# Performance work log

Hardware: AMD Instinct MI355X
Metric: run time of the kernel (lower is better)

The kernel has to match this reference:

```python
import jax, jax.numpy as jnp
import numpy as np

B, T, D = 2, 2048, 2048
H, KV, HD = 16, 4, 128
EPS = 1e-6


def _rmsnorm(x, scale):
    # flax.linen.RMSNorm over last axis: x / sqrt(mean(x^2) + eps) * scale
    var = jnp.mean(jnp.square(x), axis=-1, keepdims=True)
    return x * jax.lax.rsqrt(var + EPS) * scale


def _rope(x, cos, sin):
    # x: [b, t, h, d]; cos/sin: [t, d]
    x_rot = jnp.stack([-x[..., 1::2], x[..., 0::2]], axis=-1)
    x_rot = x_rot.reshape(*x_rot.shape[:-2], -1)
    return x * cos[None, :, None, :] + x_rot * sin[None, :, None, :]


def setup_inputs() -> dict:
    key = jax.random.key(0)
    ks = jax.random.split(key, 5)
    x = jax.random.normal(ks[0], (B, T, D), jnp.float32)
    Wq = jax.random.normal(ks[1], (D, H * HD), jnp.float32) / np.sqrt(D)
    Wk = jax.random.normal(ks[2], (D, KV * HD), jnp.float32) / np.sqrt(D)
    Wv = jax.random.normal(ks[3], (D, KV * HD), jnp.float32) / np.sqrt(D)
    Wo = jax.random.normal(ks[4], (H * HD, D), jnp.float32) / np.sqrt(H * HD)
    q_scale = jnp.ones((HD,), jnp.float32)
    k_scale = jnp.ones((HD,), jnp.float32)
    # standard RoPE tables, interleaved-pair convention
    pos = jnp.arange(T, dtype=jnp.float32)
    inv_freq = 1.0 / (10000.0 ** (jnp.arange(0, HD, 2, dtype=jnp.float32) / HD))
    freqs = pos[:, None] * inv_freq[None, :]  # [T, HD/2]
    cos = jnp.repeat(jnp.cos(freqs), 2, axis=-1)  # [T, HD]
    sin = jnp.repeat(jnp.sin(freqs), 2, axis=-1)
    mask = jnp.tril(jnp.ones((T, T), bool))[None, None]  # causal [1,1,T,T]
    return {"x": x, "Wq": Wq, "Wk": Wk, "Wv": Wv, "Wo": Wo,
            "q_scale": q_scale, "k_scale": k_scale,
            "cos": cos, "sin": sin, "mask": mask}


def reference(x, Wq, Wk, Wv, Wo, q_scale, k_scale, cos, sin, mask):
    num_groups = H // KV
    q = (x @ Wq).reshape(B, T, H, HD)
    k = (x @ Wk).reshape(B, T, KV, HD)
    v = (x @ Wv).reshape(B, T, KV, HD)
    q = _rmsnorm(q, q_scale)
    k = _rmsnorm(k, k_scale)
    q = _rope(q, cos, sin)
    k = _rope(k, cos, sin)
    k = jnp.repeat(k, num_groups, axis=2)  # [b, t, H, d]
    v = jnp.repeat(v, num_groups, axis=2)
    scores = jnp.einsum('bqhd,bkhd->bhqk', q, k) / jnp.sqrt(jnp.float32(HD))
    scores = jnp.where(mask, scores, jnp.finfo(scores.dtype).min)
    attn = jax.nn.softmax(scores, axis=-1)
    out = jnp.einsum('bhqk,bkhd->bqhd', attn, v)
    out = out.reshape(B, T, H * HD)
    return out @ Wo
```

## Files before the change

### kernel.cpp

```cpp
#include <hip/hip_runtime.h>
#include <hip/hip_bf16.h>

#define B_   2
#define T_   2048
#define D_   2048
#define H_   16
#define KV_  4
#define HD_  128
#define BT_  (B_*T_)
#define QKVP 3072
#define KOFF 2048
#define VOFF 2560
static constexpr float EPS_ = 1e-6f;

typedef unsigned short u16;
typedef __attribute__((ext_vector_type(8))) short short8;
typedef __attribute__((ext_vector_type(4))) float f32x4;
typedef __attribute__((ext_vector_type(4))) unsigned short u16x4;

__device__ __forceinline__ u16 f2bf(float f){
    unsigned u = __float_as_uint(f);
    u += 0x7FFF + ((u >> 16) & 1);
    return (u16)(u >> 16);
}
__device__ __forceinline__ float bf2f(u16 u){
    return __uint_as_float((unsigned)u << 16);
}

__device__ __forceinline__ void async_copy16(const void* g, void* l) {
    __builtin_amdgcn_global_load_lds(
        (const __attribute__((address_space(1))) unsigned int*)g,
        (__attribute__((address_space(3))) unsigned int*)l, 16, 0, 0);
}

__global__ __launch_bounds__(256) void cvt_f32_bf16_kernel(
    const float* __restrict__ in, u16* __restrict__ out, int n)
{
    const int i = (blockIdx.x*256 + threadIdx.x)*4;
    if (i < n) {
        float4 v = *(const float4*)&in[i];
        u16x4 w = { f2bf(v.x), f2bf(v.y), f2bf(v.z), f2bf(v.w) };
        *(u16x4*)&out[i] = w;
    }
}

__global__ __launch_bounds__(256) void transpose_cvt_kernel(
    const float* __restrict__ in, u16* __restrict__ out, int R, int C)
{
    __shared__ u16 tile[64][65];
    const int r0 = blockIdx.y*64, c0 = blockIdx.x*64;
    const int tr = threadIdx.x >> 4;
    const int tc = (threadIdx.x & 15) * 4;
    #pragma unroll
    for (int i = 0; i < 4; i++) {
        const int r = tr + i*16;
        float4 v = *(const float4*)&in[(size_t)(r0 + r)*C + c0 + tc];
        tile[tc+0][r] = f2bf(v.x);
        tile[tc+1][r] = f2bf(v.y);
        tile[tc+2][r] = f2bf(v.z);
        tile[tc+3][r] = f2bf(v.w);
    }
    __syncthreads();
    #pragma unroll
    for (int i = 0; i < 4; i++) {
        const int c = tr + i*16;
        u16x4 w = { tile[c][tc+0], tile[c][tc+1], tile[c][tc+2], tile[c][tc+3] };
        *(u16x4*)&out[(size_t)(c0 + c)*R + r0 + tc] = w;
    }
}

__global__ __launch_bounds__(256) void transpose_v_kernel(
    const u16* __restrict__ qkv, u16* __restrict__ vt)
{
    __shared__ u16 tile[64][65];
    const int t0 = blockIdx.x*64;
    const int d0 = blockIdx.y*64;
    const int bk = blockIdx.z;
    const int tr = threadIdx.x >> 4;
    const int tc = (threadIdx.x & 15) * 4;
    #pragma unroll
    for (int i = 0; i < 4; i++) {
        const int t = t0 + tr + i*16;
        u16x4 v = *(const u16x4*)&qkv[(size_t)((bk>>2)*T_ + t)*QKVP + VOFF
                                      + (bk&3)*HD_ + d0 + tc];
        tile[tc+0][tr+i*16] = v[0];
        tile[tc+1][tr+i*16] = v[1];
        tile[tc+2][tr+i*16] = v[2];
        tile[tc+3][tr+i*16] = v[3];
    }
    __syncthreads();
    #pragma unroll
    for (int i = 0; i < 4; i++) {
        const int d = tr + i*16;
        u16x4 w = { tile[d][tc+0], tile[d][tc+1], tile[d][tc+2], tile[d][tc+3] };
        *(u16x4*)&vt[((size_t)bk*HD_ + d0 + d)*T_ + t0 + tc] = w;
    }
}

#define GBM 128
#define GBN 128
#define GBK 32

template<bool OUT_BF16>
__global__ __launch_bounds__(256) void gemm_mfma_kernel(
    const u16* __restrict__ A, const u16* __restrict__ Bt,
    void* __restrict__ C, int N, int K, int lda, int ldb, int ldc)
{
    __shared__ __align__(16) u16 As[GBM][GBK];
    __shared__ __align__(16) u16 Bs[GBN][GBK];
    const int tid  = threadIdx.x;
    const int lane = tid & 63;
    const int wave = tid >> 6;
    const int l15  = lane & 15;
    const int quad = lane >> 4;
    const int wr   = (wave >> 1) * 64;
    const int wc   = (wave & 1) * 64;
    const size_t row0 = (size_t)blockIdx.y * GBM;
    const size_t col0 = (size_t)blockIdx.x * GBN;

    f32x4 acc[4][4];
    #pragma unroll
    for (int i = 0; i < 4; i++)
        #pragma unroll
        for (int j = 0; j < 4; j++)
            acc[i][j] = (f32x4){0.f,0.f,0.f,0.f};

    for (int k0 = 0; k0 < K; k0 += GBK) {
        #pragma unroll
        for (int c = 0; c < 2; c++) {
            const int e = (c*256 + tid) * 8;
            const int r = e >> 5, cc = e & 31;
            async_copy16(A  + (row0 + r)*lda + k0 + cc, &As[r][cc]);
            async_copy16(Bt + (col0 + r)*ldb + k0 + cc, &Bs[r][cc]);
        }
        __syncthreads();

        short8 af[4], bf[4];
        #pragma unroll
        for (int i = 0; i < 4; i++)
            af[i] = *(const short8*)&As[wr + i*16 + l15][quad*8];
        #pragma unroll
        for (int j = 0; j < 4; j++)
            bf[j] = *(const short8*)&Bs[wc + j*16 + l15][quad*8];
        #pragma unroll
        for (int i = 0; i < 4; i++)
            #pragma unroll
            for (int j = 0; j < 4; j++)
                acc[i][j] = __builtin_amdgcn_mfma_f32_16x16x32_bf16(
                    af[i], bf[j], acc[i][j], 0, 0, 0);
        __syncthreads();
    }

    #pragma unroll
    for (int i = 0; i < 4; i++)
        #pragma unroll
        for (int r = 0; r < 4; r++) {
            const size_t row = row0 + wr + i*16 + quad*4 + r;
            #pragma unroll
            for (int j = 0; j < 4; j++) {
                const size_t col = col0 + wc + j*16 + l15;
                if (OUT_BF16) ((u16*)C)[row*ldc + col] = f2bf(acc[i][j][r]);
                else          ((float*)C)[row*ldc + col] = acc[i][j][r];
            }
        }
}

__global__ __launch_bounds__(256) void rmsnorm_rope_kernel(
    u16* __restrict__ qk, const float* __restrict__ scale,
    const float* __restrict__ cosT, const float* __restrict__ sinT,
    int heads_per_token, int head_off, float post_scale)
{
    const int wid   = blockIdx.x*4 + (threadIdx.x >> 6);
    const int lane  = threadIdx.x & 63;
    const int token = wid / heads_per_token;
    const int hidx  = wid % heads_per_token;
    const int t     = token & (T_ - 1);
    u16* p = qk + (size_t)token*QKVP + head_off + hidx*HD_ + lane*2;

    const unsigned u = *(const unsigned*)p;
    const float x0 = bf2f((u16)(u & 0xffff));
    const float x1 = bf2f((u16)(u >> 16));
    float ss = x0*x0 + x1*x1;
    #pragma unroll
    for (int off = 32; off > 0; off >>= 1) ss += __shfl_xor(ss, off);
    const float rms = rsqrtf(ss * (1.0f/HD_) + EPS_);

    const float2 sc = *(const float2*)&scale[lane*2];
    const float2 cs = *(const float2*)&cosT[(size_t)t*HD_ + lane*2];
    const float2 sn = *(const float2*)&sinT[(size_t)t*HD_ + lane*2];
    const float n0 = x0 * rms * sc.x;
    const float n1 = x1 * rms * sc.y;
    const float r0 = (n0*cs.x - n1*sn.x) * post_scale;
    const float r1 = (n1*cs.y + n0*sn.y) * post_scale;
    *(unsigned*)p = (unsigned)f2bf(r0) | ((unsigned)f2bf(r1) << 16);
}

#define BQ2 128
#define BKV 64

__global__ __launch_bounds__(256, 2) void attn_mfma12_kernel(
    const u16* __restrict__ qkv, const u16* __restrict__ Vtg)
{
    __shared__ __align__(16) u16 Ks[2][16][BKV][8];
    __shared__ __align__(16) u16 Vt[2][8][HD_][8];
    __shared__ __align__(16) u16 Pb[4][2][8][16][8];

    const int x    = blockIdx.x;
    const int h    = blockIdx.y;
    const int b    = blockIdx.z;
    const int qt   = b ? x : 15 - x;
    const int kvh  = h >> 2;
    const int tid  = threadIdx.x;
    const int lane = tid & 63;
    const int wave = tid >> 6;
    const int l15  = lane & 15;
    const int quad = lane >> 4;
    const int q0   = qt * BQ2;
    const int ntiles = 2*qt + 2;

    short8 qf[2][4];
    #pragma unroll
    for (int rf = 0; rf < 2; rf++) {
        const u16* qbase = qkv + (size_t)(b*T_ + q0 + rf*64 + wave*16 + l15)*QKVP + h*HD_;
        #pragma unroll
        for (int kt = 0; kt < 4; kt++)
            qf[rf][kt] = *(const short8*)(qbase + kt*32 + quad*8);
    }

    float lsum[2][4];
    #pragma unroll
    for (int rf = 0; rf < 2; rf++)
        #pragma unroll
        for (int r = 0; r < 4; r++) lsum[rf][r] = 0.f;
    f32x4 oacc[2][8];
    #pragma unroll
    for (int rf = 0; rf < 2; rf++)
        #pragma unroll
        for (int cv = 0; cv < 8; cv++) oacc[rf][cv] = (f32x4){0.f,0.f,0.f,0.f};

    #pragma unroll
    for (int it = 0; it < 4; it++) {
        const int n2  = it*256 + tid;
        const int cc  = n2 >> 6;
        const int key = n2 & 63;
        async_copy16(qkv + (size_t)(b*T_ + key)*QKVP + KOFF + kvh*HD_ + cc*8,
                     &Ks[0][cc][key][0]);
    }
    #pragma unroll
    for (int it = 0; it < 4; it++) {
        const int n2 = it*256 + tid;
        const int cc = n2 >> 7;
        const int d  = n2 & 127;
        async_copy16(Vtg + ((size_t)(b*KV_ + kvh)*HD_ + d)*T_ + cc*8,
                     &Vt[0][cc][d][0]);
    }
    __syncthreads();

    int cur = 0;
    for (int t = 0; t < ntiles; t++) {
        if (t + 1 < ntiles) {
            const int k0n = (t + 1) * BKV;
            #pragma unroll
            for (int it = 0; it < 4; it++) {
                const int n2  = it*256 + tid;
                const int cc  = n2 >> 6;
                const int key = n2 & 63;
                async_copy16(qkv + (size_t)(b*T_ + k0n + key)*QKVP + KOFF + kvh*HD_ + cc*8,
                             &Ks[cur^1][cc][key][0]);
            }
            #pragma unroll
            for (int it = 0; it < 4; it++) {
                const int n2 = it*256 + tid;
                const int cc = n2 >> 7;
                const int d  = n2 & 127;
                async_copy16(Vtg + ((size_t)(b*KV_ + kvh)*HD_ + d)*T_ + k0n + cc*8,
                             &Vt[cur^1][cc][d][0]);
            }
        }

        const int k0 = t * BKV;

        f32x4 s[2][4];
        #pragma unroll
        for (int rf = 0; rf < 2; rf++)
            #pragma unroll
            for (int c = 0; c < 4; c++) s[rf][c] = (f32x4){0.f,0.f,0.f,0.f};
        __builtin_amdgcn_s_setprio(1);
        #pragma unroll
        for (int kt = 0; kt < 4; kt++) {
            #pragma unroll
            for (int c = 0; c < 4; c++) {
                short8 kf = *(const short8*)&Ks[cur][kt*4 + quad][c*16 + l15][0];
                #pragma unroll
                for (int rf = 0; rf < 2; rf++)
                    s[rf][c] = __builtin_amdgcn_mfma_f32_16x16x32_bf16(
                        qf[rf][kt], kf, s[rf][c], 0, 0, 0);
            }
        }
        __builtin_amdgcn_s_setprio(0);

        if (t >= ntiles - 2) {
            #pragma unroll
            for (int rf = 0; rf < 2; rf++) {
                const int qrow0 = q0 + rf*64 + wave*16 + quad*4;
                #pragma unroll
                for (int r = 0; r < 4; r++)
                    #pragma unroll
                    for (int c = 0; c < 4; c++) {
                        const int key = k0 + c*16 + l15;
                        if (key > qrow0 + r) s[rf][c][r] = -1e30f;
                    }
            }
        }
        #pragma unroll
        for (int rf = 0; rf < 2; rf++)
            #pragma unroll
            for (int r = 0; r < 4; r++)
                #pragma unroll
                for (int c = 0; c < 4; c++) {
                    const float p = __expf(s[rf][c][r]);
                    lsum[rf][r] += p;
                    Pb[wave][rf][c*2 + (l15 >> 3)][quad*4 + r][l15 & 7] = f2bf(p);
                }

        __builtin_amdgcn_s_setprio(1);
        #pragma unroll
        for (int kt2 = 0; kt2 < 2; kt2++) {
            short8 pa[2];
            #pragma unroll
            for (int rf = 0; rf < 2; rf++)
                pa[rf] = *(const short8*)&Pb[wave][rf][kt2*4 + quad][l15][0];
            #pragma unroll
            for (int cv = 0; cv < 8; cv++) {
                short8 vf = *(const short8*)&Vt[cur][kt2*4 + quad][cv*16 + l15][0];
                #pragma unroll
                for (int rf = 0; rf < 2; rf++)
                    oacc[rf][cv] = __builtin_amdgcn_mfma_f32_16x16x32_bf16(
                        pa[rf], vf, oacc[rf][cv], 0, 0, 0);
            }
        }
        __builtin_amdgcn_s_setprio(0);

        __syncthreads();
        cur ^= 1;
    }

    #pragma unroll
    for (int rf = 0; rf < 2; rf++)
        #pragma unroll
        for (int r = 0; r < 4; r++) {
            float tot = lsum[rf][r];
            #pragma unroll
            for (int off = 1; off < 16; off <<= 1)
                tot += __shfl_xor(tot, off, 16);
            const float linv = 1.0f / tot;
            u16* orow = (u16*)qkv + (size_t)(b*T_ + q0 + rf*64 + wave*16 + quad*4 + r)*QKVP
                        + h*HD_ + l15;
            #pragma unroll
            for (int cv = 0; cv < 8; cv++)
                orow[cv*16] = f2bf(oacc[rf][cv][r] * linv);
        }
}

extern "C" void kernel_launch(void* const* d_in, const int* in_sizes, int n_in,
                              void* d_out, int out_size, void* d_ws, size_t ws_size,
                              hipStream_t stream)
{
    const float* x    = (const float*)d_in[0];
    const float* Wq   = (const float*)d_in[1];
    const float* Wk   = (const float*)d_in[2];
    const float* Wv   = (const float*)d_in[3];
    const float* Wo   = (const float*)d_in[4];
    const float* qsc  = (const float*)d_in[5];
    const float* ksc  = (const float*)d_in[6];
    const float* cosT = (const float*)d_in[7];
    const float* sinT = (const float*)d_in[8];
    float* out = (float*)d_out;

    u16* xb     = (u16*)d_ws;
    u16* Wqkvt  = xb    + (size_t)BT_*D_;
    u16* Wot    = Wqkvt + (size_t)QKVP*D_;
    u16* qkv    = Wot   + (size_t)D_*(H_*HD_);
    u16* vtg    = qkv   + (size_t)BT_*QKVP;

    cvt_f32_bf16_kernel<<<(BT_*D_)/1024, 256, 0, stream>>>(x, xb, BT_*D_);
    transpose_cvt_kernel<<<dim3((H_*HD_)/64,  D_/64), 256, 0, stream>>>(
        Wq, Wqkvt, D_, H_*HD_);
    transpose_cvt_kernel<<<dim3((KV_*HD_)/64, D_/64), 256, 0, stream>>>(
        Wk, Wqkvt + (size_t)KOFF*D_, D_, KV_*HD_);
    transpose_cvt_kernel<<<dim3((KV_*HD_)/64, D_/64), 256, 0, stream>>>(
        Wv, Wqkvt + (size_t)VOFF*D_, D_, KV_*HD_);
    transpose_cvt_kernel<<<dim3(D_/64, (H_*HD_)/64),  256, 0, stream>>>(
        Wo, Wot, H_*HD_, D_);

    gemm_mfma_kernel<true><<<dim3(QKVP/GBN, BT_/GBM), 256, 0, stream>>>(
        xb, Wqkvt, qkv, QKVP, D_, D_, D_, QKVP);

    rmsnorm_rope_kernel<<<(BT_*H_)/4,  256, 0, stream>>>(
        qkv, qsc, cosT, sinT, H_, 0, 0.08838834764831845f);
    rmsnorm_rope_kernel<<<(BT_*KV_)/4, 256, 0, stream>>>(
        qkv, ksc, cosT, sinT, KV_, KOFF, 1.0f);

    transpose_v_kernel<<<dim3(T_/64, HD_/64, B_*KV_), 256, 0, stream>>>(qkv, vtg);

    attn_mfma12_kernel<<<dim3(T_/BQ2, H_, B_), 256, 0, stream>>>(qkv, vtg);

    gemm_mfma_kernel<false><<<dim3(D_/GBN, BT_/GBM), 256, 0, stream>>>(
        qkv, Wot, out, D_, D_, QKVP, D_, D_);
}
```

Before: 380.1 us.

## Split long causal query tiles across two KV halves with combine pass

The eight longest causal query tiles per head are each split into two blocks, one per half of the KV range. Each half writes unnormalized fp32 partial outputs and row sums, and a new combine kernel adds the halves, normalizes and writes bf16. The goal is to shorten the critical path of the attention grid and improve load balance across CUs. The cost is an extra launch plus fp32 partial traffic, staged in the output buffer and the x-bf16 workspace. Plain summation of the halves is only correct because the softmax uses a fixed max rather than a running one.

```diff
diff --git a/kernel.cpp b/kernel.cpp
--- a/kernel.cpp
+++ b/kernel.cpp
@@ -197,18 +197,35 @@
 
 #define BQ2 128
 #define BKV 64
-
-__global__ __launch_bounds__(256, 2) void attn_mfma12_kernel(
-    const u16* __restrict__ qkv, const u16* __restrict__ Vtg)
+#define QSPLIT   8
+#define NSPL     8
+#define POTILE   (128*128)
+
+__global__ __launch_bounds__(256, 2) void attn_mfma13_kernel(
+    const u16* __restrict__ qkv, const u16* __restrict__ Vtg,
+    float* __restrict__ partO, float* __restrict__ psum)
 {
     __shared__ __align__(16) u16 Ks[2][16][BKV][8];
     __shared__ __align__(16) u16 Vt[2][8][HD_][8];
     __shared__ __align__(16) u16 Pb[4][2][8][16][8];
 
-    const int x    = blockIdx.x;
+    const int xb2  = blockIdx.x;
     const int h    = blockIdx.y;
     const int b    = blockIdx.z;
-    const int qt   = b ? x : 15 - x;
+    int qt, t0, t1, half;
+    bool full;
+    if (xb2 < 2*NSPL) {
+        qt   = 15 - (xb2 >> 1);
+        half = xb2 & 1;
+        t0   = half ? (qt + 1) : 0;
+        t1   = half ? (2*qt + 2) : (qt + 1);
+        full = false;
+    } else {
+        qt   = 23 - xb2;
+        t0   = 0; t1 = 2*qt + 2; half = 0;
+        full = true;
+    }
+
     const int kvh  = h >> 2;
     const int tid  = threadIdx.x;
     const int lane = tid & 63;
@@ -216,7 +233,6 @@
     const int l15  = lane & 15;
     const int quad = lane >> 4;
     const int q0   = qt * BQ2;
-    const int ntiles = 2*qt + 2;
 
     short8 qf[2][4];
     #pragma unroll
@@ -238,27 +254,30 @@
         #pragma unroll
         for (int cv = 0; cv < 8; cv++) oacc[rf][cv] = (f32x4){0.f,0.f,0.f,0.f};
 
-    #pragma unroll
-    for (int it = 0; it < 4; it++) {
-        const int n2  = it*256 + tid;
-        const int cc  = n2 >> 6;
-        const int key = n2 & 63;
-        async_copy16(qkv + (size_t)(b*T_ + key)*QKVP + KOFF + kvh*HD_ + cc*8,
-                     &Ks[0][cc][key][0]);
-    }
-    #pragma unroll
-    for (int it = 0; it < 4; it++) {
-        const int n2 = it*256 + tid;
-        const int cc = n2 >> 7;
-        const int d  = n2 & 127;
-        async_copy16(Vtg + ((size_t)(b*KV_ + kvh)*HD_ + d)*T_ + cc*8,
-                     &Vt[0][cc][d][0]);
+    {
+        const int k00 = t0 * BKV;
+        #pragma unroll
+        for (int it = 0; it < 4; it++) {
+            const int n2  = it*256 + tid;
+            const int cc  = n2 >> 6;
+            const int key = n2 & 63;
+            async_copy16(qkv + (size_t)(b*T_ + k00 + key)*QKVP + KOFF + kvh*HD_ + cc*8,
+                         &Ks[0][cc][key][0]);
+        }
+        #pragma unroll
+        for (int it = 0; it < 4; it++) {
+            const int n2 = it*256 + tid;
+            const int cc = n2 >> 7;
+            const int d  = n2 & 127;
+            async_copy16(Vtg + ((size_t)(b*KV_ + kvh)*HD_ + d)*T_ + k00 + cc*8,
+                         &Vt[0][cc][d][0]);
+        }
     }
     __syncthreads();
 
     int cur = 0;
-    for (int t = 0; t < ntiles; t++) {
-        if (t + 1 < ntiles) {
+    for (int t = t0; t < t1; t++) {
+        if (t + 1 < t1) {
             const int k0n = (t + 1) * BKV;
             #pragma unroll
             for (int it = 0; it < 4; it++) {
@@ -299,7 +318,7 @@
         }
         __builtin_amdgcn_s_setprio(0);
 
-        if (t >= ntiles - 2) {
+        if (t >= 2*qt) {
             #pragma unroll
             for (int rf = 0; rf < 2; rf++) {
                 const int qrow0 = q0 + rf*64 + wave*16 + quad*4;
@@ -345,21 +364,71 @@
         cur ^= 1;
     }
 
-    #pragma unroll
-    for (int rf = 0; rf < 2; rf++)
-        #pragma unroll
-        for (int r = 0; r < 4; r++) {
-            float tot = lsum[rf][r];
-            #pragma unroll
-            for (int off = 1; off < 16; off <<= 1)
-                tot += __shfl_xor(tot, off, 16);
-            const float linv = 1.0f / tot;
-            u16* orow = (u16*)qkv + (size_t)(b*T_ + q0 + rf*64 + wave*16 + quad*4 + r)*QKVP
-                        + h*HD_ + l15;
-            #pragma unroll
-            for (int cv = 0; cv < 8; cv++)
-                orow[cv*16] = f2bf(oacc[rf][cv][r] * linv);
-        }
+    if (full) {
+        #pragma unroll
+        for (int rf = 0; rf < 2; rf++)
+            #pragma unroll
+            for (int r = 0; r < 4; r++) {
+                float tot = lsum[rf][r];
+                #pragma unroll
+                for (int off = 1; off < 16; off <<= 1)
+                    tot += __shfl_xor(tot, off, 16);
+                const float linv = 1.0f / tot;
+                u16* orow = (u16*)qkv + (size_t)(b*T_ + q0 + rf*64 + wave*16 + quad*4 + r)*QKVP
+                            + h*HD_ + l15;
+                #pragma unroll
+                for (int cv = 0; cv < 8; cv++)
+                    orow[cv*16] = f2bf(oacc[rf][cv][r] * linv);
+            }
+    } else {
+        const int hidx = ((b*H_ + h)*NSPL + (qt - QSPLIT))*2 + half;
+        float* po = partO + (size_t)hidx*POTILE;
+        float* ps = psum  + (size_t)hidx*128;
+        #pragma unroll
+        for (int rf = 0; rf < 2; rf++)
+            #pragma unroll
+            for (int r = 0; r < 4; r++) {
+                float tot = lsum[rf][r];
+                #pragma unroll
+                for (int off = 1; off < 16; off <<= 1)
+                    tot += __shfl_xor(tot, off, 16);
+                const int row = rf*64 + wave*16 + quad*4 + r;
+                #pragma unroll
+                for (int cv = 0; cv < 8; cv++)
+                    po[row*128 + cv*16 + l15] = oacc[rf][cv][r];
+                if (l15 == 0) ps[row] = tot;
+            }
+    }
+}
+
+__global__ __launch_bounds__(256) void attn_combine_kernel(
+    const float* __restrict__ partO, const float* __restrict__ psum,
+    u16* __restrict__ qkv)
+{
+    const int p  = blockIdx.x;
+    const int qt = QSPLIT + (p & 7);
+    const int bh = p >> 3;
+    const int h  = bh & 15;
+    const int b  = bh >> 4;
+    const int base = ((b*H_ + h)*NSPL + (qt - QSPLIT))*2;
+    const float* p0 = partO + (size_t)(base + 0)*POTILE;
+    const float* p1 = partO + (size_t)(base + 1)*POTILE;
+    const float* s0 = psum  + (size_t)(base + 0)*128;
+    const float* s1 = psum  + (size_t)(base + 1)*128;
+    const int tid = threadIdx.x;
+    const int row = tid >> 1;
+    const int c0  = (tid & 1) * 64;
+    const float linv = 1.0f / (s0[row] + s1[row]);
+    u16* orow = qkv + (size_t)(b*T_ + qt*BQ2 + row)*QKVP + h*HD_;
+    #pragma unroll
+    for (int d = 0; d < 64; d += 4) {
+        const int col = c0 + d;
+        u16x4 w = { f2bf((p0[row*128 + col+0] + p1[row*128 + col+0]) * linv),
+                    f2bf((p0[row*128 + col+1] + p1[row*128 + col+1]) * linv),
+                    f2bf((p0[row*128 + col+2] + p1[row*128 + col+2]) * linv),
+                    f2bf((p0[row*128 + col+3] + p1[row*128 + col+3]) * linv) };
+        *(u16x4*)&orow[col] = w;
+    }
 }
 
 extern "C" void kernel_launch(void* const* d_in, const int* in_sizes, int n_in,
@@ -382,6 +451,8 @@
     u16* Wot    = Wqkvt + (size_t)QKVP*D_;
     u16* qkv    = Wot   + (size_t)D_*(H_*HD_);
     u16* vtg    = qkv   + (size_t)BT_*QKVP;
+    float* partO = out;
+    float* psum  = (float*)xb;
 
     cvt_f32_bf16_kernel<<<(BT_*D_)/1024, 256, 0, stream>>>(x, xb, BT_*D_);
     transpose_cvt_kernel<<<dim3((H_*HD_)/64,  D_/64), 256, 0, stream>>>(
@@ -403,7 +474,10 @@
 
     transpose_v_kernel<<<dim3(T_/64, HD_/64, B_*KV_), 256, 0, stream>>>(qkv, vtg);
 
-    attn_mfma12_kernel<<<dim3(T_/BQ2, H_, B_), 256, 0, stream>>>(qkv, vtg);
+    attn_mfma13_kernel<<<dim3(2*NSPL + QSPLIT, H_, B_), 256, 0, stream>>>(
+        qkv, vtg, partO, psum);
+
+    attn_combine_kernel<<<B_*H_*NSPL, 256, 0, stream>>>(partO, psum, qkv);
 
     gemm_mfma_kernel<false><<<dim3(D_/GBN, BT_/GBM), 256, 0, stream>>>(
         qkv, Wot, out, D_, D_, QKVP, D_, D_);
```

After: 398.3 us. 1.05x slower.

## Enlarge attention query tile to 256 rows with 8 waves and XOR-swizzled LDS

Applied to the files above, without the earlier changes.

The attention kernel now processes 256 query rows per block using 512 threads (8 waves), so each staged K/V tile is reused by twice as many queries. The K and V shared-memory layouts are changed to a row-major form with an XOR swizzle on the 16-byte chunk index, meant to avoid LDS bank conflicts on the fragment reads. The balanced reordering of query tiles across batches is dropped, and the grid halves to 256 blocks at one block per CU. This raises the causal tail imbalance and lowers occupancy in exchange for less K/V load traffic.

```diff
diff --git a/kernel.cpp b/kernel.cpp
--- a/kernel.cpp
+++ b/kernel.cpp
@@ -195,33 +195,32 @@
     *(unsigned*)p = (unsigned)f2bf(r0) | ((unsigned)f2bf(r1) << 16);
 }
 
-#define BQ2 128
+#define BQ3 256
 #define BKV 64
 
-__global__ __launch_bounds__(256, 2) void attn_mfma12_kernel(
+__global__ __launch_bounds__(512, 1) void attn_mfma14_kernel(
     const u16* __restrict__ qkv, const u16* __restrict__ Vtg)
 {
-    __shared__ __align__(16) u16 Ks[2][16][BKV][8];
-    __shared__ __align__(16) u16 Vt[2][8][HD_][8];
-    __shared__ __align__(16) u16 Pb[4][2][8][16][8];
-
-    const int x    = blockIdx.x;
+    __shared__ __align__(16) u16 Ks[2][BKV][16][8];
+    __shared__ __align__(16) u16 Vt[2][HD_][8][8];
+    __shared__ __align__(16) u16 Pb[8][2][8][16][8];
+
+    const int qt   = blockIdx.x;
     const int h    = blockIdx.y;
     const int b    = blockIdx.z;
-    const int qt   = b ? x : 15 - x;
     const int kvh  = h >> 2;
     const int tid  = threadIdx.x;
     const int lane = tid & 63;
     const int wave = tid >> 6;
     const int l15  = lane & 15;
     const int quad = lane >> 4;
-    const int q0   = qt * BQ2;
-    const int ntiles = 2*qt + 2;
+    const int q0   = qt * BQ3;
+    const int ntiles = 4*qt + 4;
 
     short8 qf[2][4];
     #pragma unroll
     for (int rf = 0; rf < 2; rf++) {
-        const u16* qbase = qkv + (size_t)(b*T_ + q0 + rf*64 + wave*16 + l15)*QKVP + h*HD_;
+        const u16* qbase = qkv + (size_t)(b*T_ + q0 + rf*128 + wave*16 + l15)*QKVP + h*HD_;
         #pragma unroll
         for (int kt = 0; kt < 4; kt++)
             qf[rf][kt] = *(const short8*)(qbase + kt*32 + quad*8);
@@ -238,44 +237,38 @@
         #pragma unroll
         for (int cv = 0; cv < 8; cv++) oacc[rf][cv] = (f32x4){0.f,0.f,0.f,0.f};
 
-    #pragma unroll
-    for (int it = 0; it < 4; it++) {
-        const int n2  = it*256 + tid;
-        const int cc  = n2 >> 6;
-        const int key = n2 & 63;
-        async_copy16(qkv + (size_t)(b*T_ + key)*QKVP + KOFF + kvh*HD_ + cc*8,
-                     &Ks[0][cc][key][0]);
-    }
-    #pragma unroll
-    for (int it = 0; it < 4; it++) {
-        const int n2 = it*256 + tid;
-        const int cc = n2 >> 7;
-        const int d  = n2 & 127;
-        async_copy16(Vtg + ((size_t)(b*KV_ + kvh)*HD_ + d)*T_ + cc*8,
-                     &Vt[0][cc][d][0]);
-    }
+#define STAGE_KV(BUF, K0)                                                     \
+    {                                                                         \
+        _Pragma("unroll")                                                     \
+        for (int it = 0; it < 2; it++) {                                      \
+            const int n2  = it*512 + tid;                                     \
+            const int key = n2 >> 4;                                          \
+            const int j   = n2 & 15;                                          \
+            const int ccS = j ^ (key & 7);                                    \
+            async_copy16(qkv + (size_t)(b*T_ + (K0) + key)*QKVP + KOFF        \
+                             + kvh*HD_ + ccS*8,                               \
+                         &Ks[BUF][key][j][0]);                                \
+        }                                                                     \
+        _Pragma("unroll")                                                     \
+        for (int it = 0; it < 2; it++) {                                      \
+            const int n2 = it*512 + tid;                                      \
+            const int d  = n2 >> 3;                                           \
+            const int j  = n2 & 7;                                            \
+            const int ccS = j ^ (d & 7);                                      \
+            async_copy16(Vtg + ((size_t)(b*KV_ + kvh)*HD_ + d)*T_ + (K0)      \
+                             + ccS*8,                                         \
+                         &Vt[BUF][d][j][0]);                                  \
+        }                                                                     \
+    }
+
+    STAGE_KV(0, 0)
     __syncthreads();
 
     int cur = 0;
     for (int t = 0; t < ntiles; t++) {
         if (t + 1 < ntiles) {
             const int k0n = (t + 1) * BKV;
-            #pragma unroll
-            for (int it = 0; it < 4; it++) {
-                const int n2  = it*256 + tid;
-                const int cc  = n2 >> 6;
-                const int key = n2 & 63;
-                async_copy16(qkv + (size_t)(b*T_ + k0n + key)*QKVP + KOFF + kvh*HD_ + cc*8,
-                             &Ks[cur^1][cc][key][0]);
-            }
-            #pragma unroll
-            for (int it = 0; it < 4; it++) {
-                const int n2 = it*256 + tid;
-                const int cc = n2 >> 7;
-                const int d  = n2 & 127;
-                async_copy16(Vtg + ((size_t)(b*KV_ + kvh)*HD_ + d)*T_ + k0n + cc*8,
-                             &Vt[cur^1][cc][d][0]);
-            }
+            if (cur == 0) STAGE_KV(1, k0n) else STAGE_KV(0, k0n)
         }
 
         const int k0 = t * BKV;
@@ -290,7 +283,9 @@
         for (int kt = 0; kt < 4; kt++) {
             #pragma unroll
             for (int c = 0; c < 4; c++) {
-                short8 kf = *(const short8*)&Ks[cur][kt*4 + quad][c*16 + l15][0];
+                const int key = c*16 + l15;
+                const int kc  = (kt*4 + quad) ^ (key & 7);
+                short8 kf = *(const short8*)&Ks[cur][key][kc][0];
                 #pragma unroll
                 for (int rf = 0; rf < 2; rf++)
                     s[rf][c] = __builtin_amdgcn_mfma_f32_16x16x32_bf16(
@@ -299,10 +294,10 @@
         }
         __builtin_amdgcn_s_setprio(0);
 
-        if (t >= ntiles - 2) {
+        if (t >= 4*qt) {
             #pragma unroll
             for (int rf = 0; rf < 2; rf++) {
-                const int qrow0 = q0 + rf*64 + wave*16 + quad*4;
+                const int qrow0 = q0 + rf*128 + wave*16 + quad*4;
                 #pragma unroll
                 for (int r = 0; r < 4; r++)
                     #pragma unroll
@@ -332,7 +327,9 @@
                 pa[rf] = *(const short8*)&Pb[wave][rf][kt2*4 + quad][l15][0];
             #pragma unroll
             for (int cv = 0; cv < 8; cv++) {
-                short8 vf = *(const short8*)&Vt[cur][kt2*4 + quad][cv*16 + l15][0];
+                const int d  = cv*16 + l15;
+                const int kc = (kt2*4 + quad) ^ (d & 7);
+                short8 vf = *(const short8*)&Vt[cur][d][kc][0];
                 #pragma unroll
                 for (int rf = 0; rf < 2; rf++)
                     oacc[rf][cv] = __builtin_amdgcn_mfma_f32_16x16x32_bf16(
@@ -354,12 +351,13 @@
             for (int off = 1; off < 16; off <<= 1)
                 tot += __shfl_xor(tot, off, 16);
             const float linv = 1.0f / tot;
-            u16* orow = (u16*)qkv + (size_t)(b*T_ + q0 + rf*64 + wave*16 + quad*4 + r)*QKVP
+            u16* orow = (u16*)qkv + (size_t)(b*T_ + q0 + rf*128 + wave*16 + quad*4 + r)*QKVP
                         + h*HD_ + l15;
             #pragma unroll
             for (int cv = 0; cv < 8; cv++)
                 orow[cv*16] = f2bf(oacc[rf][cv][r] * linv);
         }
+#undef STAGE_KV
 }
 
 extern "C" void kernel_launch(void* const* d_in, const int* in_sizes, int n_in,
@@ -403,7 +401,7 @@
 
     transpose_v_kernel<<<dim3(T_/64, HD_/64, B_*KV_), 256, 0, stream>>>(qkv, vtg);
 
-    attn_mfma12_kernel<<<dim3(T_/BQ2, H_, B_), 256, 0, stream>>>(qkv, vtg);
+    attn_mfma14_kernel<<<dim3(T_/BQ3, H_, B_), 512, 0, stream>>>(qkv, vtg);
 
     gemm_mfma_kernel<false><<<dim3(D_/GBN, BT_/GBM), 256, 0, stream>>>(
         qkv, Wot, out, D_, D_, QKVP, D_, D_);
```

Result: faster. 367.1 us (-3.4%).
